# Optimization experiments

Hardware: AMD Instinct MI355X
Metric: run time of the kernel (lower is better)

## Reference

```python
import jax, jax.numpy as jnp
import numpy as np

# ---- fixed wavelet filters (Selesnick FSfarras first-stage + Kingsbury Q-shift) ----
_F1 = np.array([
    [0.0, 0.0],
    [-0.08838834764832, -0.01122679215254],
    [0.08838834764832, 0.01122679215254],
    [0.69587998903400, 0.08838834764832],
    [0.69587998903400, 0.08838834764832],
    [0.08838834764832, -0.69587998903400],
    [-0.08838834764832, 0.69587998903400],
    [0.01122679215254, -0.08838834764832],
    [0.01122679215254, -0.08838834764832],
    [0.0, 0.0]], np.float32)
_F2 = np.array([
    [0.01122679215254, 0.0],
    [0.01122679215254, 0.0],
    [-0.08838834764832, -0.08838834764832],
    [0.08838834764832, -0.08838834764832],
    [0.69587998903400, 0.69587998903400],
    [0.69587998903400, -0.69587998903400],
    [0.08838834764832, 0.08838834764832],
    [-0.08838834764832, 0.08838834764832],
    [0.0, 0.01122679215254],
    [0.0, -0.01122679215254]], np.float32)
_Q1 = np.array([
    [0.03516384, 0.0],
    [0.0, 0.0],
    [-0.08832942, -0.11430184],
    [0.23389032, 0.0],
    [0.76027237, 0.58751830],
    [0.58751830, -0.76027237],
    [0.0, 0.23389032],
    [-0.11430184, 0.08832942],
    [0.0, 0.0],
    [0.0, -0.03516384]], np.float32)
_Q2 = np.array([
    [0.0, -0.03516384],
    [0.0, 0.0],
    [-0.11430184, 0.08832942],
    [0.0, 0.23389032],
    [0.58751830, -0.76027237],
    [0.76027237, 0.58751830],
    [0.23389032, 0.0],
    [-0.08832942, -0.11430184],
    [0.0, 0.0],
    [0.03516384, 0.0]], np.float32)
# synthesis filters are the time-reversed analysis filters
FSF = jnp.asarray(np.stack([_F1[::-1].copy(), _F2[::-1].copy()]))  # [2, 10, 2] first stage
SF = jnp.asarray(np.stack([_Q1[::-1].copy(), _Q2[::-1].copy()]))   # [2, 10, 2] Q-shift


def _upconv(x, f, axis):
    """Upsample-by-2 + full convolution with 1D filter f along `axis` (upfirdn(x,f,2,1))."""
    L = f.shape[0]
    xm = jnp.moveaxis(x, axis, -1)
    shp = xm.shape
    xr = xm.reshape(-1, 1, shp[-1])  # [M, 1, n] NCW
    k = f[::-1].astype(x.dtype).reshape(1, 1, L)  # flip -> true convolution
    y = jax.lax.conv_general_dilated(
        xr, k, window_strides=(1,), padding=[(L - 1, L - 1)],
        lhs_dilation=(2,), dimension_numbers=('NCW', 'OIW', 'NCW'))  # [M,1,2n+L-2]
    y = y.reshape(shp[:-1] + (y.shape[-1],))
    return jnp.moveaxis(y, -1, axis)


def sfb1d(lo, hi, sf, axis):
    """1D synthesis filter bank with periodic wrap + circular shift (Selesnick sfb1D)."""
    L = sf.shape[0]
    N = 2 * lo.shape[axis]
    y = _upconv(lo, sf[:, 0], axis) + _upconv(hi, sf[:, 1], axis)  # length N+L-2
    yN = jax.lax.slice_in_dim(y, 0, N, axis=axis)
    tail = jax.lax.slice_in_dim(y, N, N + L - 2, axis=axis)
    head = jax.lax.slice_in_dim(yN, 0, L - 2, axis=axis) + tail
    rest = jax.lax.slice_in_dim(yN, L - 2, N, axis=axis)
    return jnp.roll(jnp.concatenate([head, rest], axis=axis), 1 - L // 2, axis=axis)


def sfb2d(lo, hi3, sf_row, sf_col):
    """2D separable synthesis: hi3 = (LH, HL, HH); x is [B, H, W, C]."""
    lo = sfb1d(lo, hi3[0], sf_col, axis=2)
    h = sfb1d(hi3[1], hi3[2], sf_col, axis=2)
    return sfb1d(lo, h, sf_row, axis=1)


def _idtcwt(highs0, highs1, lows):
    inv_sqrt2 = jnp.asarray(1.0 / np.sqrt(2.0), highs0.dtype)

    def pm(a, b):
        return (a + b) * inv_sqrt2, (a - b) * inv_sqrt2

    # orientation butterflies per level (add_sub)
    wi = [[[[None] * 3 for _ in range(2)] for _ in range(2)] for _ in range(2)]
    for j, hj in enumerate((highs0, highs1)):
        for b in range(3):
            u, v = pm(hj[0, 0, b], hj[1, 1, b])
            wi[j][0][0][b], wi[j][1][1][b] = u, v
            u, v = pm(hj[0, 1, b], hj[1, 0, b])
            wi[j][0][1][b], wi[j][1][0][b] = u, v

    y = jnp.zeros_like(lows[0, 0], shape=(lows.shape[2], lows.shape[3] * 4,
                                          lows.shape[4] * 4, lows.shape[5]))
    for m in range(2):
        for n in range(2):
            lo = lows[m, n]
            lo = sfb2d(lo, wi[1][m][n], SF[m], SF[n])      # level 2 (Q-shift)
            lo = sfb2d(lo, wi[0][m][n], FSF[m], FSF[n])    # level 1 (first stage)
            y = y + lo
    return y / 2


def setup_inputs() -> dict:
    key = jax.random.key(0)
    k0, k1, k2 = jax.random.split(key, 3)
    B, C = 16, 3
    highs0 = jax.random.normal(k0, (2, 2, 3, B, 256, 256, C), dtype=jnp.float32)
    highs1 = jax.random.normal(k1, (2, 2, 3, B, 128, 128, C), dtype=jnp.float32)
    lows = jax.random.normal(k2, (2, 2, B, 128, 128, C), dtype=jnp.float32)
    return {"highs0": highs0, "highs1": highs1, "lows": lows}


def reference(highs0, highs1, lows):
    return _idtcwt(highs0, highs1, lows)
```

## Files before the change

### kernel.cpp

```cpp
#include <hip/hip_runtime.h>

#define INV_SQRT2 0.70710678118654752440f
#define KH 0.35355339059327376220f

constexpr float c_first[2][10][2] = {
  { { 0.00000000000000f,  0.00000000000000f},
    {-0.08838834764832f, -0.01122679215254f},
    { 0.08838834764832f,  0.01122679215254f},
    { 0.69587998903400f,  0.08838834764832f},
    { 0.69587998903400f,  0.08838834764832f},
    { 0.08838834764832f, -0.69587998903400f},
    {-0.08838834764832f,  0.69587998903400f},
    { 0.01122679215254f, -0.08838834764832f},
    { 0.01122679215254f, -0.08838834764832f},
    { 0.00000000000000f,  0.00000000000000f} },
  { { 0.01122679215254f,  0.00000000000000f},
    { 0.01122679215254f,  0.00000000000000f},
    {-0.08838834764832f, -0.08838834764832f},
    { 0.08838834764832f, -0.08838834764832f},
    { 0.69587998903400f,  0.69587998903400f},
    { 0.69587998903400f, -0.69587998903400f},
    { 0.08838834764832f,  0.08838834764832f},
    {-0.08838834764832f,  0.08838834764832f},
    { 0.00000000000000f,  0.01122679215254f},
    { 0.00000000000000f, -0.01122679215254f} }
};

__constant__ float c_qshift[2][10][2] = {
  { { 0.03516384f,  0.00000000f},
    { 0.00000000f,  0.00000000f},
    {-0.08832942f, -0.11430184f},
    { 0.23389032f,  0.00000000f},
    { 0.76027237f,  0.58751830f},
    { 0.58751830f, -0.76027237f},
    { 0.00000000f,  0.23389032f},
    {-0.11430184f,  0.08832942f},
    { 0.00000000f,  0.00000000f},
    { 0.00000000f, -0.03516384f} },
  { { 0.00000000f, -0.03516384f},
    { 0.00000000f,  0.00000000f},
    {-0.11430184f,  0.08832942f},
    { 0.00000000f,  0.23389032f},
    { 0.58751830f, -0.76027237f},
    { 0.76027237f,  0.58751830f},
    { 0.23389032f,  0.00000000f},
    {-0.08832942f, -0.11430184f},
    { 0.00000000f,  0.00000000f},
    { 0.03516384f,  0.00000000f} }
};

__global__ __launch_bounds__(128, 3) void idtcwt_stage1(
    const float* __restrict__ lows, const float* __restrict__ highs1,
    float* __restrict__ lo2)
{
  constexpr int HIN = 128, WIN = 128, C = 3, B = 16;
  constexpr int ROWF  = WIN * C;
  constexpr int ROWO  = 2 * WIN * C;
  constexpr int PLANE = HIN * WIN * C;
  constexpr int SEG   = 16;

  const int jj = blockIdx.x * 128 + threadIdx.x;
  const int c  = jj % 3;
  const int t  = jj / 3;
  const int z  = blockIdx.z;
  const int combo = z >> 4;
  const int b     = z & 15;
  const int m = combo >> 1, n = combo & 1;

  const float* lo = lows + (combo * B + b) * PLANE;
  const int pa = (m == n) ? 0 : 1;
  const int pb = (m == n) ? 3 : 2;
  const float sgn = (m == 0) ? 1.0f : -1.0f;
  const int bandStride = B * PLANE;
  const float* hA = highs1 + (pa * 3 * B + b) * PLANE;
  const float* hB = highs1 + (pb * 3 * B + b) * PLANE;

  int wc3[5];
#pragma unroll
  for (int p = 0; p < 5; ++p) {
    int w = t + 2 - p;
    if (w >= WIN) w -= WIN;
    if (w < 0)  w += WIN;
    wc3[p] = w * C + c;
  }

  float lae[5], lao[5], hae[5], hao[5];
#pragma unroll
  for (int k = 0; k < 5; ++k) { lae[k]=0.f; lao[k]=0.f; hae[k]=0.f; hao[k]=0.f; }

  const int s0 = blockIdx.y * SEG;
  float* outp = lo2 + (combo * B + b) * (4 * PLANE);

#pragma unroll 1
  for (int ui = 0; ui < SEG + 4; ++ui) {
    const int u  = (s0 - 2 + ui) & (HIN - 1);
#pragma unroll
    for (int k = 0; k < 4; ++k) { lae[k]=lae[k+1]; lao[k]=lao[k+1]; hae[k]=hae[k+1]; hao[k]=hao[k+1]; }
    const int rb = u * ROWF;

    float rl[5], rA[3][5], rB[3][5];
#pragma unroll
    for (int p = 0; p < 5; ++p) {
      const int idx = rb + wc3[p];
      rl[p]    = lo[idx];
      rA[0][p] = hA[idx];
      rB[0][p] = hB[idx];
      rA[1][p] = hA[idx +   bandStride];
      rB[1][p] = hB[idx +   bandStride];
      rA[2][p] = hA[idx + 2*bandStride];
      rB[2][p] = hB[idx + 2*bandStride];
    }
    asm volatile("" :: "v"(rl[0]),"v"(rl[1]),"v"(rl[2]),"v"(rl[3]),"v"(rl[4]),
                       "v"(rA[0][0]),"v"(rA[0][1]),"v"(rA[0][2]),"v"(rA[0][3]),"v"(rA[0][4]),
                       "v"(rA[1][0]),"v"(rA[1][1]),"v"(rA[1][2]),"v"(rA[1][3]),"v"(rA[1][4]));
    asm volatile("" :: "v"(rA[2][0]),"v"(rA[2][1]),"v"(rA[2][2]),"v"(rA[2][3]),"v"(rA[2][4]),
                       "v"(rB[0][0]),"v"(rB[0][1]),"v"(rB[0][2]),"v"(rB[0][3]),"v"(rB[0][4]),
                       "v"(rB[1][0]),"v"(rB[1][1]),"v"(rB[1][2]),"v"(rB[1][3]),"v"(rB[1][4]));
    asm volatile("" :: "v"(rB[2][0]),"v"(rB[2][1]),"v"(rB[2][2]),"v"(rB[2][3]),"v"(rB[2][4]));

    float aLe=0.f, aLo=0.f, aHe=0.f, aHo=0.f;
#pragma unroll
    for (int p = 0; p < 5; ++p) {
      const float lv  = rl[p];
      const float lhv = (rA[0][p] + sgn * rB[0][p]) * INV_SQRT2;
      const float hlv = (rA[1][p] + sgn * rB[1][p]) * INV_SQRT2;
      const float hhv = (rA[2][p] + sgn * rB[2][p]) * INV_SQRT2;
      const float ce0 = c_qshift[n][9 - 2*p][0], ce1 = c_qshift[n][9 - 2*p][1];
      const float co0 = c_qshift[n][8 - 2*p][0], co1 = c_qshift[n][8 - 2*p][1];
      aLe += ce0 * lv  + ce1 * lhv;
      aLo += co0 * lv  + co1 * lhv;
      aHe += ce0 * hlv + ce1 * hhv;
      aHo += co0 * hlv + co1 * hhv;
    }
    lae[4]=aLe; lao[4]=aLo; hae[4]=aHe; hao[4]=aHo;

    if (ui >= 4) {
      const int s = s0 + ui - 4;
      float o00=0.f, o01=0.f, o10=0.f, o11=0.f;
#pragma unroll
      for (int p = 0; p < 5; ++p) {
        const float f0l = c_qshift[m][9 - 2*p][0], f0h = c_qshift[m][9 - 2*p][1];
        const float f1l = c_qshift[m][8 - 2*p][0], f1h = c_qshift[m][8 - 2*p][1];
        o00 += f0l*lae[4-p] + f0h*hae[4-p];
        o01 += f0l*lao[4-p] + f0h*hao[4-p];
        o10 += f1l*lae[4-p] + f1h*hae[4-p];
        o11 += f1l*lao[4-p] + f1h*hao[4-p];
      }
      float* q = outp + (2*s) * ROWO + (2*t) * C + c;
      q[0]        = o00;
      q[C]        = o01;
      q[ROWO]     = o10;
      q[ROWO + C] = o11;
    }
  }
}

__global__ __launch_bounds__(256, 4) void idtcwt_stage2(
    const float* __restrict__ lo2, const float* __restrict__ highs0,
    float* __restrict__ out)
{
  constexpr int HIN = 256, WIN = 256, C = 3, B = 16;
  constexpr int ROWF  = WIN * C;
  constexpr int ROWO  = 2 * WIN * C;
  constexpr int PLANE = HIN * WIN * C;
  constexpr int OPLANE = 512 * 512 * C;
  constexpr int SEG   = 8;
  constexpr int NI    = SEG + 4;
  constexpr int PITCH = 5;
  constexpr int BUFV4 = 272 * PITCH;
  constexpr int LDSV4 = 3072;

  __shared__ float4 lds4[LDSV4];

  const int tid = threadIdx.x;
  const int jj  = blockIdx.x * 256 + tid;
  const int c   = jj % 3;
  const int t   = jj / 3;
  const int b   = blockIdx.z;

  const int bandStride = B * PLANE;
  const float* a0  = lo2 + (0 * B + b) * PLANE;
  const float* a1  = lo2 + (1 * B + b) * PLANE;
  const float* a2  = lo2 + (2 * B + b) * PLANE;
  const float* a3  = lo2 + (3 * B + b) * PLANE;
  const float* h00b0 = highs0 + (0 * 3 * B + b) * PLANE;
  const float* h01b0 = highs0 + (1 * 3 * B + b) * PLANE;
  const float* h10b0 = highs0 + (2 * 3 * B + b) * PLANE;
  const float* h11b0 = highs0 + (3 * 3 * B + b) * PLANE;
  const float* h00b1 = h00b0 + bandStride;
  const float* h01b1 = h01b0 + bandStride;
  const float* h10b1 = h10b0 + bandStride;
  const float* h11b1 = h11b0 + bandStride;
  const float* h00b2 = h00b0 + 2*bandStride;
  const float* h01b2 = h01b0 + 2*bandStride;
  const float* h10b2 = h10b0 + 2*bandStride;
  const float* h11b2 = h11b0 + 2*bandStride;

  int j1 = jj - 6;   if (j1 < 0)     j1 += ROWF;
  int j2 = jj + 250; if (j2 >= ROWF) j2 -= ROWF;
  const bool halo = (tid < 12);

  float wla0e[6], wla0o[6], wla1e[6], wla1o[6];
  float wha0e[6], wha0o[6], wha1e[6], wha1o[6];
#pragma unroll
  for (int k = 0; k < 6; ++k) {
    wla0e[k]=0.f; wla0o[k]=0.f; wla1e[k]=0.f; wla1o[k]=0.f;
    wha0e[k]=0.f; wha0o[k]=0.f; wha1e[k]=0.f; wha1o[k]=0.f;
  }

  const int s0 = blockIdx.y * SEG;
  float* outb = out + b * OPLANE;

  float4 G0, G1, G2, G3;
  float4 Hh0 = make_float4(0.f,0.f,0.f,0.f), Hh1 = Hh0, Hh2 = Hh0, Hh3 = Hh0;

#define S2_LOAD(I)                                                           \
  {                                                                          \
    const int rb_ = ((s0 - 2 + (I)) & (HIN - 1)) * ROWF;                     \
    const int o1_ = rb_ + j1;                                                \
    G0 = make_float4(a0[o1_], a1[o1_], a2[o1_], a3[o1_]);                    \
    G1 = make_float4(h00b0[o1_], h11b0[o1_], h01b0[o1_], h10b0[o1_]);        \
    G2 = make_float4(h00b1[o1_], h11b1[o1_], h01b1[o1_], h10b1[o1_]);        \
    G3 = make_float4(h00b2[o1_], h11b2[o1_], h01b2[o1_], h10b2[o1_]);        \
    if (halo) {                                                              \
      const int o2_ = rb_ + j2;                                              \
      Hh0 = make_float4(a0[o2_], a1[o2_], a2[o2_], a3[o2_]);                 \
      Hh1 = make_float4(h00b0[o2_], h11b0[o2_], h01b0[o2_], h10b0[o2_]);     \
      Hh2 = make_float4(h00b1[o2_], h11b1[o2_], h01b1[o2_], h10b1[o2_]);     \
      Hh3 = make_float4(h00b2[o2_], h11b2[o2_], h01b2[o2_], h10b2[o2_]);     \
    }                                                                        \
  }

#define S2_WRITE()                                                           \
  {                                                                          \
    float4* w_ = lds4 + tid * PITCH;                                         \
    w_[0] = make_float4(G0.x*0.5f, G0.y*0.5f, G0.z*0.5f, G0.w*0.5f);         \
    w_[1] = make_float4((G1.x+G1.y)*KH, (G1.x-G1.y)*KH,                      \
                        (G1.z+G1.w)*KH, (G1.z-G1.w)*KH);                     \
    w_[2] = make_float4((G2.x+G2.y)*KH, (G2.x-G2.y)*KH,                      \
                        (G2.z+G2.w)*KH, (G2.z-G2.w)*KH);                     \
    w_[3] = make_float4((G3.x+G3.y)*KH, (G3.x-G3.y)*KH,                      \
                        (G3.z+G3.w)*KH, (G3.z-G3.w)*KH);                     \
    if (halo) {                                                              \
      float4* w2_ = lds4 + (256 + tid) * PITCH;                              \
      w2_[0] = make_float4(Hh0.x*0.5f, Hh0.y*0.5f, Hh0.z*0.5f, Hh0.w*0.5f);  \
      w2_[1] = make_float4((Hh1.x+Hh1.y)*KH, (Hh1.x-Hh1.y)*KH,               \
                           (Hh1.z+Hh1.w)*KH, (Hh1.z-Hh1.w)*KH);              \
      w2_[2] = make_float4((Hh2.x+Hh2.y)*KH, (Hh2.x-Hh2.y)*KH,               \
                           (Hh2.z+Hh2.w)*KH, (Hh2.z-Hh2.w)*KH);              \
      w2_[3] = make_float4((Hh3.x+Hh3.y)*KH, (Hh3.x-Hh3.y)*KH,               \
                           (Hh3.z+Hh3.w)*KH, (Hh3.z-Hh3.w)*KH);              \
    }                                                                        \
  }

  S2_LOAD(0);
  S2_WRITE();
  __syncthreads();

#pragma unroll 1
  for (int uo = 0; uo < 2; ++uo) {
#pragma unroll
    for (int k = 0; k < 6; ++k) {
      const int i = uo * 6 + k;

      if (i < NI - 1) {
        S2_LOAD(i + 1);
        __builtin_amdgcn_sched_barrier(0);
      }

      float A0e=0.f,A0o=0.f,A1e=0.f,A1o=0.f, H0e=0.f,H0o=0.f,H1e=0.f,H1o=0.f;
#pragma unroll
      for (int p = 0; p < 5; ++p) {
        const float4* qp = lds4 + (tid + (12 - 3*p)) * PITCH;
        const float4 q0 = qp[0], q1 = qp[1], q2 = qp[2], q3 = qp[3];
        const float a0e = c_first[0][9-2*p][0], a0o = c_first[0][8-2*p][0];
        const float b0e = c_first[0][9-2*p][1], b0o = c_first[0][8-2*p][1];
        const float a1e = c_first[1][9-2*p][0], a1o = c_first[1][8-2*p][0];
        const float b1e = c_first[1][9-2*p][1], b1o = c_first[1][8-2*p][1];
        A0e += a0e*q0.x + a1e*q0.y;   A0o += a0o*q0.x + a1o*q0.y;
        A1e += a0e*q0.z + a1e*q0.w;   A1o += a0o*q0.z + a1o*q0.w;
        A0e += b0e*q1.x + b1e*q1.z;   A0o += b0o*q1.x + b1o*q1.z;
        A1e += b0e*q1.w + b1e*q1.y;   A1o += b0o*q1.w + b1o*q1.y;
        H0e += a0e*q2.x + a1e*q2.z;   H0o += a0o*q2.x + a1o*q2.z;
        H1e += a0e*q2.w + a1e*q2.y;   H1o += a0o*q2.w + a1o*q2.y;
        H0e += b0e*q3.x + b1e*q3.z;   H0o += b0o*q3.x + b1o*q3.z;
        H1e += b0e*q3.w + b1e*q3.y;   H1o += b0o*q3.w + b1o*q3.y;
      }
      wla0e[k]=A0e; wla0o[k]=A0o; wla1e[k]=A1e; wla1o[k]=A1o;
      wha0e[k]=H0e; wha0o[k]=H0o; wha1e[k]=H1e; wha1o[k]=H1o;

      if (i >= 4) {
        const int s = s0 + i - 4;
        float o00=0.f, o01=0.f, o10=0.f, o11=0.f;
#pragma unroll
        for (int p = 0; p < 5; ++p) {
          const int kk = (k - p + 6) % 6;
          const float f00 = c_first[0][9-2*p][0], g00 = c_first[0][9-2*p][1];
          const float f01 = c_first[0][8-2*p][0], g01 = c_first[0][8-2*p][1];
          const float f10 = c_first[1][9-2*p][0], g10 = c_first[1][9-2*p][1];
          const float f11 = c_first[1][8-2*p][0], g11 = c_first[1][8-2*p][1];
          o00 += f00*wla0e[kk] + g00*wha0e[kk] + f10*wla1e[kk] + g10*wha1e[kk];
          o01 += f00*wla0o[kk] + g00*wha0o[kk] + f10*wla1o[kk] + g10*wha1o[kk];
          o10 += f01*wla0e[kk] + g01*wha0e[kk] + f11*wla1e[kk] + g11*wha1e[kk];
          o11 += f01*wla0o[kk] + g01*wha0o[kk] + f11*wla1o[kk] + g11*wha1o[kk];
        }
        float* q = outb + (2*s) * ROWO + (2*t) * C + c;
        q[0]        = o00;
        q[C]        = o01;
        q[ROWO]     = o10;
        q[ROWO + C] = o11;
      }

      __syncthreads();
      if (i < NI - 1) {
        S2_WRITE();
      }
      __syncthreads();
    }
  }
#undef S2_LOAD
#undef S2_WRITE
}

extern "C" void kernel_launch(void* const* d_in, const int* in_sizes, int n_in,
                              void* d_out, int out_size, void* d_ws, size_t ws_size,
                              hipStream_t stream) {
  const float* highs0 = (const float*)d_in[0];
  const float* highs1 = (const float*)d_in[1];
  const float* lows   = (const float*)d_in[2];
  float* out = (float*)d_out;
  float* lo2 = (float*)d_ws;

  dim3 b1(128), g1(3, 8, 64);
  hipLaunchKernelGGL(idtcwt_stage1, g1, b1, 0, stream, lows, highs1, lo2);

  dim3 b2(256), g2(3, 32, 16);
  hipLaunchKernelGGL(idtcwt_stage2, g2, b2, 0, stream, lo2, highs0, out);
}
```

Baseline: 119.8 us.

## Process two rows per barrier pair and double stage-2 row segment

Stage 2 now handles 16 output rows per block instead of 8, which shrinks the 4-row halo recompute overhead relative to useful work. It also loads, transforms and filters two input rows per iteration into two LDS halves, halving the number of __syncthreads pairs. The rolling window is cut from 6 to 5 entries. In exchange there is higher register pressure from double-buffered loads, and half as many blocks in the grid, which lowers parallelism.

```diff
diff --git a/kernel.cpp b/kernel.cpp
--- a/kernel.cpp
+++ b/kernel.cpp
@@ -164,10 +164,9 @@
   constexpr int ROWO  = 2 * WIN * C;
   constexpr int PLANE = HIN * WIN * C;
   constexpr int OPLANE = 512 * 512 * C;
-  constexpr int SEG   = 8;
-  constexpr int NI    = SEG + 4;
+  constexpr int SEG   = 16;
   constexpr int PITCH = 5;
-  constexpr int BUFV4 = 272 * PITCH;
+  constexpr int HALF  = 272 * PITCH;
   constexpr int LDSV4 = 3072;
 
   __shared__ float4 lds4[LDSV4];
@@ -200,10 +199,10 @@
   int j2 = jj + 250; if (j2 >= ROWF) j2 -= ROWF;
   const bool halo = (tid < 12);
 
-  float wla0e[6], wla0o[6], wla1e[6], wla1o[6];
-  float wha0e[6], wha0o[6], wha1e[6], wha1o[6];
-#pragma unroll
-  for (int k = 0; k < 6; ++k) {
+  float wla0e[5], wla0o[5], wla1e[5], wla1o[5];
+  float wha0e[5], wha0o[5], wha1e[5], wha1o[5];
+#pragma unroll
+  for (int k = 0; k < 5; ++k) {
     wla0e[k]=0.f; wla0o[k]=0.f; wla1e[k]=0.f; wla1o[k]=0.f;
     wha0e[k]=0.f; wha0o[k]=0.f; wha1e[k]=0.f; wha1o[k]=0.f;
   }
@@ -211,115 +210,129 @@
   const int s0 = blockIdx.y * SEG;
   float* outb = out + b * OPLANE;
 
-  float4 G0, G1, G2, G3;
-  float4 Hh0 = make_float4(0.f,0.f,0.f,0.f), Hh1 = Hh0, Hh2 = Hh0, Hh3 = Hh0;
-
-#define S2_LOAD(I)                                                           \
+  float4 GA0, GA1, GA2, GA3;
+  float4 GAh0 = make_float4(0,0,0,0), GAh1 = GAh0, GAh2 = GAh0, GAh3 = GAh0;
+  float4 GB0, GB1, GB2, GB3;
+  float4 GBh0 = make_float4(0,0,0,0), GBh1 = GBh0, GBh2 = GBh0, GBh3 = GBh0;
+
+#define S2_LOADR(I, g0,g1,g2,g3, hh0,hh1,hh2,hh3)                            \
   {                                                                          \
     const int rb_ = ((s0 - 2 + (I)) & (HIN - 1)) * ROWF;                     \
     const int o1_ = rb_ + j1;                                                \
-    G0 = make_float4(a0[o1_], a1[o1_], a2[o1_], a3[o1_]);                    \
-    G1 = make_float4(h00b0[o1_], h11b0[o1_], h01b0[o1_], h10b0[o1_]);        \
-    G2 = make_float4(h00b1[o1_], h11b1[o1_], h01b1[o1_], h10b1[o1_]);        \
-    G3 = make_float4(h00b2[o1_], h11b2[o1_], h01b2[o1_], h10b2[o1_]);        \
+    g0 = make_float4(a0[o1_], a1[o1_], a2[o1_], a3[o1_]);                    \
+    g1 = make_float4(h00b0[o1_], h11b0[o1_], h01b0[o1_], h10b0[o1_]);        \
+    g2 = make_float4(h00b1[o1_], h11b1[o1_], h01b1[o1_], h10b1[o1_]);        \
+    g3 = make_float4(h00b2[o1_], h11b2[o1_], h01b2[o1_], h10b2[o1_]);        \
     if (halo) {                                                              \
       const int o2_ = rb_ + j2;                                              \
-      Hh0 = make_float4(a0[o2_], a1[o2_], a2[o2_], a3[o2_]);                 \
-      Hh1 = make_float4(h00b0[o2_], h11b0[o2_], h01b0[o2_], h10b0[o2_]);     \
-      Hh2 = make_float4(h00b1[o2_], h11b1[o2_], h01b1[o2_], h10b1[o2_]);     \
-      Hh3 = make_float4(h00b2[o2_], h11b2[o2_], h01b2[o2_], h10b2[o2_]);     \
+      hh0 = make_float4(a0[o2_], a1[o2_], a2[o2_], a3[o2_]);                 \
+      hh1 = make_float4(h00b0[o2_], h11b0[o2_], h01b0[o2_], h10b0[o2_]);     \
+      hh2 = make_float4(h00b1[o2_], h11b1[o2_], h01b1[o2_], h10b1[o2_]);     \
+      hh3 = make_float4(h00b2[o2_], h11b2[o2_], h01b2[o2_], h10b2[o2_]);     \
     }                                                                        \
   }
 
-#define S2_WRITE()                                                           \
+#define S2_WRITER(HOFF, g0,g1,g2,g3, hh0,hh1,hh2,hh3)                        \
   {                                                                          \
-    float4* w_ = lds4 + tid * PITCH;                                         \
-    w_[0] = make_float4(G0.x*0.5f, G0.y*0.5f, G0.z*0.5f, G0.w*0.5f);         \
-    w_[1] = make_float4((G1.x+G1.y)*KH, (G1.x-G1.y)*KH,                      \
-                        (G1.z+G1.w)*KH, (G1.z-G1.w)*KH);                     \
-    w_[2] = make_float4((G2.x+G2.y)*KH, (G2.x-G2.y)*KH,                      \
-                        (G2.z+G2.w)*KH, (G2.z-G2.w)*KH);                     \
-    w_[3] = make_float4((G3.x+G3.y)*KH, (G3.x-G3.y)*KH,                      \
-                        (G3.z+G3.w)*KH, (G3.z-G3.w)*KH);                     \
+    float4* w_ = lds4 + (HOFF) + tid * PITCH;                                \
+    w_[0] = make_float4(g0.x*0.5f, g0.y*0.5f, g0.z*0.5f, g0.w*0.5f);         \
+    w_[1] = make_float4((g1.x+g1.y)*KH, (g1.x-g1.y)*KH,                      \
+                        (g1.z+g1.w)*KH, (g1.z-g1.w)*KH);                     \
+    w_[2] = make_float4((g2.x+g2.y)*KH, (g2.x-g2.y)*KH,                      \
+                        (g2.z+g2.w)*KH, (g2.z-g2.w)*KH);                     \
+    w_[3] = make_float4((g3.x+g3.y)*KH, (g3.x-g3.y)*KH,                      \
+                        (g3.z+g3.w)*KH, (g3.z-g3.w)*KH);                     \
     if (halo) {                                                              \
-      float4* w2_ = lds4 + (256 + tid) * PITCH;                              \
-      w2_[0] = make_float4(Hh0.x*0.5f, Hh0.y*0.5f, Hh0.z*0.5f, Hh0.w*0.5f);  \
-      w2_[1] = make_float4((Hh1.x+Hh1.y)*KH, (Hh1.x-Hh1.y)*KH,               \
-                           (Hh1.z+Hh1.w)*KH, (Hh1.z-Hh1.w)*KH);              \
-      w2_[2] = make_float4((Hh2.x+Hh2.y)*KH, (Hh2.x-Hh2.y)*KH,               \
-                           (Hh2.z+Hh2.w)*KH, (Hh2.z-Hh2.w)*KH);              \
-      w2_[3] = make_float4((Hh3.x+Hh3.y)*KH, (Hh3.x-Hh3.y)*KH,               \
-                           (Hh3.z+Hh3.w)*KH, (Hh3.z-Hh3.w)*KH);              \
+      float4* w2_ = lds4 + (HOFF) + (256 + tid) * PITCH;                     \
+      w2_[0] = make_float4(hh0.x*0.5f, hh0.y*0.5f, hh0.z*0.5f, hh0.w*0.5f);  \
+      w2_[1] = make_float4((hh1.x+hh1.y)*KH, (hh1.x-hh1.y)*KH,               \
+                           (hh1.z+hh1.w)*KH, (hh1.z-hh1.w)*KH);              \
+      w2_[2] = make_float4((hh2.x+hh2.y)*KH, (hh2.x-hh2.y)*KH,               \
+                           (hh2.z+hh2.w)*KH, (hh2.z-hh2.w)*KH);              \
+      w2_[3] = make_float4((hh3.x+hh3.y)*KH, (hh3.x-hh3.y)*KH,               \
+                           (hh3.z+hh3.w)*KH, (hh3.z-hh3.w)*KH);              \
     }                                                                        \
   }
 
-  S2_LOAD(0);
-  S2_WRITE();
+#define S2_COL(HOFF, KS, IVAL)                                               \
+  {                                                                          \
+    float A0e=0.f,A0o=0.f,A1e=0.f,A1o=0.f, H0e=0.f,H0o=0.f,H1e=0.f,H1o=0.f;  \
+    _Pragma("unroll")                                                        \
+    for (int p = 0; p < 5; ++p) {                                            \
+      const float4* qp = lds4 + (HOFF) + (tid + (12 - 3*p)) * PITCH;         \
+      const float4 q0 = qp[0], q1 = qp[1], q2 = qp[2], q3 = qp[3];           \
+      const float a0e_ = c_first[0][9-2*p][0], a0o_ = c_first[0][8-2*p][0];  \
+      const float b0e_ = c_first[0][9-2*p][1], b0o_ = c_first[0][8-2*p][1];  \
+      const float a1e_ = c_first[1][9-2*p][0], a1o_ = c_first[1][8-2*p][0];  \
+      const float b1e_ = c_first[1][9-2*p][1], b1o_ = c_first[1][8-2*p][1];  \
+      A0e += a0e_*q0.x + a1e_*q0.y;   A0o += a0o_*q0.x + a1o_*q0.y;          \
+      A1e += a0e_*q0.z + a1e_*q0.w;   A1o += a0o_*q0.z + a1o_*q0.w;          \
+      A0e += b0e_*q1.x + b1e_*q1.z;   A0o += b0o_*q1.x + b1o_*q1.z;          \
+      A1e += b0e_*q1.w + b1e_*q1.y;   A1o += b0o_*q1.w + b1o_*q1.y;          \
+      H0e += a0e_*q2.x + a1e_*q2.z;   H0o += a0o_*q2.x + a1o_*q2.z;          \
+      H1e += a0e_*q2.w + a1e_*q2.y;   H1o += a0o_*q2.w + a1o_*q2.y;          \
+      H0e += b0e_*q3.x + b1e_*q3.z;   H0o += b0o_*q3.x + b1o_*q3.z;          \
+      H1e += b0e_*q3.w + b1e_*q3.y;   H1o += b0o_*q3.w + b1o_*q3.y;          \
+    }                                                                        \
+    wla0e[KS]=A0e; wla0o[KS]=A0o; wla1e[KS]=A1e; wla1o[KS]=A1o;              \
+    wha0e[KS]=H0e; wha0o[KS]=H0o; wha1e[KS]=H1e; wha1o[KS]=H1o;              \
+    if ((IVAL) >= 4) {                                                       \
+      const int s_ = s0 + (IVAL) - 4;                                        \
+      float o00=0.f, o01=0.f, o10=0.f, o11=0.f;                              \
+      _Pragma("unroll")                                                      \
+      for (int p = 0; p < 5; ++p) {                                          \
+        const int kk = ((KS) - p + 5) % 5;                                   \
+        const float f00 = c_first[0][9-2*p][0], g00 = c_first[0][9-2*p][1];  \
+        const float f01 = c_first[0][8-2*p][0], g01 = c_first[0][8-2*p][1];  \
+        const float f10 = c_first[1][9-2*p][0], g10 = c_first[1][9-2*p][1];  \
+        const float f11 = c_first[1][8-2*p][0], g11 = c_first[1][8-2*p][1];  \
+        o00 += f00*wla0e[kk] + g00*wha0e[kk] + f10*wla1e[kk] + g10*wha1e[kk];\
+        o01 += f00*wla0o[kk] + g00*wha0o[kk] + f10*wla1o[kk] + g10*wha1o[kk];\
+        o10 += f01*wla0e[kk] + g01*wha0e[kk] + f11*wla1e[kk] + g11*wha1e[kk];\
+        o11 += f01*wla0o[kk] + g01*wha0o[kk] + f11*wla1o[kk] + g11*wha1o[kk];\
+      }                                                                      \
+      float* q_ = outb + (2*s_) * ROWO + (2*t) * C + c;                      \
+      q_[0]        = o00;                                                    \
+      q_[C]        = o01;                                                    \
+      q_[ROWO]     = o10;                                                    \
+      q_[ROWO + C] = o11;                                                    \
+    }                                                                        \
+  }
+
+  S2_LOADR(0, GA0,GA1,GA2,GA3, GAh0,GAh1,GAh2,GAh3);
+  S2_LOADR(1, GB0,GB1,GB2,GB3, GBh0,GBh1,GBh2,GBh3);
+  S2_WRITER(0,    GA0,GA1,GA2,GA3, GAh0,GAh1,GAh2,GAh3);
+  S2_WRITER(HALF, GB0,GB1,GB2,GB3, GBh0,GBh1,GBh2,GBh3);
   __syncthreads();
 
 #pragma unroll 1
   for (int uo = 0; uo < 2; ++uo) {
 #pragma unroll
-    for (int k = 0; k < 6; ++k) {
-      const int i = uo * 6 + k;
-
-      if (i < NI - 1) {
-        S2_LOAD(i + 1);
+    for (int jp = 0; jp < 5; ++jp) {
+      const int jph = uo * 5 + jp;
+      const int i0  = 2 * jph;
+      const int i1  = i0 + 1;
+
+      if (jph < 9) {
+        S2_LOADR(i0 + 2, GA0,GA1,GA2,GA3, GAh0,GAh1,GAh2,GAh3);
+        S2_LOADR(i1 + 2, GB0,GB1,GB2,GB3, GBh0,GBh1,GBh2,GBh3);
         __builtin_amdgcn_sched_barrier(0);
       }
 
-      float A0e=0.f,A0o=0.f,A1e=0.f,A1o=0.f, H0e=0.f,H0o=0.f,H1e=0.f,H1o=0.f;
-#pragma unroll
-      for (int p = 0; p < 5; ++p) {
-        const float4* qp = lds4 + (tid + (12 - 3*p)) * PITCH;
-        const float4 q0 = qp[0], q1 = qp[1], q2 = qp[2], q3 = qp[3];
-        const float a0e = c_first[0][9-2*p][0], a0o = c_first[0][8-2*p][0];
-        const float b0e = c_first[0][9-2*p][1], b0o = c_first[0][8-2*p][1];
-        const float a1e = c_first[1][9-2*p][0], a1o = c_first[1][8-2*p][0];
-        const float b1e = c_first[1][9-2*p][1], b1o = c_first[1][8-2*p][1];
-        A0e += a0e*q0.x + a1e*q0.y;   A0o += a0o*q0.x + a1o*q0.y;
-        A1e += a0e*q0.z + a1e*q0.w;   A1o += a0o*q0.z + a1o*q0.w;
-        A0e += b0e*q1.x + b1e*q1.z;   A0o += b0o*q1.x + b1o*q1.z;
-        A1e += b0e*q1.w + b1e*q1.y;   A1o += b0o*q1.w + b1o*q1.y;
-        H0e += a0e*q2.x + a1e*q2.z;   H0o += a0o*q2.x + a1o*q2.z;
-        H1e += a0e*q2.w + a1e*q2.y;   H1o += a0o*q2.w + a1o*q2.y;
-        H0e += b0e*q3.x + b1e*q3.z;   H0o += b0o*q3.x + b1o*q3.z;
-        H1e += b0e*q3.w + b1e*q3.y;   H1o += b0o*q3.w + b1o*q3.y;
-      }
-      wla0e[k]=A0e; wla0o[k]=A0o; wla1e[k]=A1e; wla1o[k]=A1o;
-      wha0e[k]=H0e; wha0o[k]=H0o; wha1e[k]=H1e; wha1o[k]=H1o;
-
-      if (i >= 4) {
-        const int s = s0 + i - 4;
-        float o00=0.f, o01=0.f, o10=0.f, o11=0.f;
-#pragma unroll
-        for (int p = 0; p < 5; ++p) {
-          const int kk = (k - p + 6) % 6;
-          const float f00 = c_first[0][9-2*p][0], g00 = c_first[0][9-2*p][1];
-          const float f01 = c_first[0][8-2*p][0], g01 = c_first[0][8-2*p][1];
-          const float f10 = c_first[1][9-2*p][0], g10 = c_first[1][9-2*p][1];
-          const float f11 = c_first[1][8-2*p][0], g11 = c_first[1][8-2*p][1];
-          o00 += f00*wla0e[kk] + g00*wha0e[kk] + f10*wla1e[kk] + g10*wha1e[kk];
-          o01 += f00*wla0o[kk] + g00*wha0o[kk] + f10*wla1o[kk] + g10*wha1o[kk];
-          o10 += f01*wla0e[kk] + g01*wha0e[kk] + f11*wla1e[kk] + g11*wha1e[kk];
-          o11 += f01*wla0o[kk] + g01*wha0o[kk] + f11*wla1o[kk] + g11*wha1o[kk];
-        }
-        float* q = outb + (2*s) * ROWO + (2*t) * C + c;
-        q[0]        = o00;
-        q[C]        = o01;
-        q[ROWO]     = o10;
-        q[ROWO + C] = o11;
-      }
+      S2_COL(0,    (2*jp) % 5,     i0);
+      S2_COL(HALF, (2*jp + 1) % 5, i1);
 
       __syncthreads();
-      if (i < NI - 1) {
-        S2_WRITE();
+      if (jph < 9) {
+        S2_WRITER(0,    GA0,GA1,GA2,GA3, GAh0,GAh1,GAh2,GAh3);
+        S2_WRITER(HALF, GB0,GB1,GB2,GB3, GBh0,GBh1,GBh2,GBh3);
       }
       __syncthreads();
     }
   }
-#undef S2_LOAD
-#undef S2_WRITE
+#undef S2_LOADR
+#undef S2_WRITER
+#undef S2_COL
 }
 
 extern "C" void kernel_launch(void* const* d_in, const int* in_sizes, int n_in,
@@ -334,6 +347,6 @@
   dim3 b1(128), g1(3, 8, 64);
   hipLaunchKernelGGL(idtcwt_stage1, g1, b1, 0, stream, lows, highs1, lo2);
 
-  dim3 b2(256), g2(3, 32, 16);
+  dim3 b2(256), g2(3, 16, 16);
   hipLaunchKernelGGL(idtcwt_stage2, g2, b2, 0, stream, lo2, highs0, out);
 }
```

Result: slower. 131.9 us (+10.1%).
